# Kernel tuning notes

Hardware: AMD Instinct MI355X
Metric: run time of the kernel (lower is better)

## Reference

```python
import jax, jax.numpy as jnp
import numpy as np

B, T, E, H = 8, 1024, 1024, 16
D = E // H  # head_dim = 64


def setup_inputs() -> dict:
    key = jax.random.key(0)
    ks = jax.random.split(key, 11)
    s = 1.0 / np.sqrt(E)
    inp = {
        'query': jax.random.normal(ks[0], (B, T, E), jnp.float32),
        'key': jax.random.normal(ks[1], (B, T, E), jnp.float32),
        'value': jax.random.normal(ks[2], (B, T, E), jnp.float32),
        'Wq': jax.random.uniform(ks[3], (E, E), jnp.float32, -s, s),
        'bq': jax.random.uniform(ks[4], (E,), jnp.float32, -s, s),
        'Wk': jax.random.uniform(ks[5], (E, E), jnp.float32, -s, s),
        'bk': jax.random.uniform(ks[6], (E,), jnp.float32, -s, s),
        'Wv': jax.random.uniform(ks[7], (E, E), jnp.float32, -s, s),
        'bv': jax.random.uniform(ks[8], (E,), jnp.float32, -s, s),
        'Wo': jax.random.uniform(ks[9], (E, E), jnp.float32, -s, s),
        'bo': jax.random.uniform(ks[10], (E,), jnp.float32, -s, s),
    }
    return inp


def reference(query, key, value, Wq, bq, Wk, bk, Wv, bv, Wo, bo):
    scale = np.sqrt(D).astype(np.float32)
    # projections: Linear applies x @ W.T + b (torch convention); W shape (out,in)
    q = (query @ Wq.T + bq).reshape(B, T, H, D).transpose(0, 2, 1, 3)  # (B,H,Tq,D)
    k = (key @ Wk.T + bk).reshape(B, T, H, D).transpose(0, 2, 1, 3)    # (B,H,Tk,D)
    v = (value @ Wv.T + bv).reshape(B, T, H, D).transpose(0, 2, 1, 3)  # (B,H,Tk,D)
    scores = jnp.einsum('bhqd,bhkd->bhqk', q, k) / scale
    attn = jax.nn.softmax(scores, axis=-1)  # dropout = identity (eval)
    out = jnp.einsum('bhqk,bhkd->bhqd', attn, v)
    out = out.transpose(0, 2, 1, 3).reshape(B, T, E)
    return out @ Wo.T + bo
```

## Files before the change

kernel.cpp:

```cpp
#include <hip/hip_runtime.h>
#include <stdint.h>

#define BB 8
#define TT 1024
#define EE 1024
#define HH 16
#define DD 64

#define L2E8 0.18033688011112042f

typedef __attribute__((ext_vector_type(8))) __bf16 bf16x8;
typedef __attribute__((ext_vector_type(4))) float f32x4;
typedef __attribute__((ext_vector_type(4))) unsigned short ushort4v;
typedef __attribute__((ext_vector_type(4))) unsigned int uint4v;

__device__ __forceinline__ unsigned short f2bf(float f) {
  unsigned int u = __float_as_uint(f);
  u += 0x7fffu + ((u >> 16) & 1u);
  return (unsigned short)(u >> 16);
}

__device__ __forceinline__ unsigned int pk2t(float a, float b) {
  return __builtin_amdgcn_perm(__float_as_uint(b) + 0x8000u,
                               __float_as_uint(a) + 0x8000u, 0x07060302u);
}

__device__ __forceinline__ f32x4 mfma_16x16x32(bf16x8 a, bf16x8 b, f32x4 c) {
  return __builtin_amdgcn_mfma_f32_16x16x32_bf16(a, b, c, 0, 0, 0);
}

__device__ __forceinline__ void async_ld16(const unsigned short* g, unsigned short* l) {
  __builtin_amdgcn_global_load_lds(
      (const __attribute__((address_space(1))) void*)g,
      (__attribute__((address_space(3))) void*)l, 16, 0, 0);
}

__global__ __launch_bounds__(256) void cast_all(
    const float* __restrict__ xq, const float* __restrict__ xk, const float* __restrict__ xv,
    const float* __restrict__ wq, const float* __restrict__ wk,
    const float* __restrict__ wv, const float* __restrict__ wo,
    unsigned short* __restrict__ ws) {
  int blk = blockIdx.x;
  const float* src; size_t dstoff; int rel;
  if (blk < 4096)       { src = xq; dstoff = 0;        rel = blk; }
  else if (blk < 8192)  { src = xk; dstoff = 8388608;  rel = blk - 4096; }
  else if (blk < 12288) { src = xv; dstoff = 16777216; rel = blk - 8192; }
  else if (blk < 12800) { src = wq; dstoff = 25165824; rel = blk - 12288; }
  else if (blk < 13312) { src = wk; dstoff = 26214400; rel = blk - 12800; }
  else if (blk < 13824) { src = wv; dstoff = 27262976; rel = blk - 13312; }
  else                  { src = wo; dstoff = 28311552; rel = blk - 13824; }
  size_t base = (size_t)rel * 2048 + (size_t)threadIdx.x * 8;
  float4 a = *(const float4*)(src + base);
  float4 b = *(const float4*)(src + base + 4);
  ushort4v o0, o1;
  o0.x = f2bf(a.x); o0.y = f2bf(a.y); o0.z = f2bf(a.z); o0.w = f2bf(a.w);
  o1.x = f2bf(b.x); o1.y = f2bf(b.y); o1.z = f2bf(b.z); o1.w = f2bf(b.w);
  *(ushort4v*)(ws + dstoff + base) = o0;
  *(ushort4v*)(ws + dstoff + base + 4) = o1;
}

__global__ __launch_bounds__(256, 3) void fused_proj(
    const unsigned short* __restrict__ xq, const unsigned short* __restrict__ xk,
    const unsigned short* __restrict__ xv, const unsigned short* __restrict__ wq,
    const unsigned short* __restrict__ wk, const unsigned short* __restrict__ wv,
    const float* __restrict__ bq, const float* __restrict__ bk, const float* __restrict__ bv,
    unsigned short* __restrict__ Qb, unsigned short* __restrict__ Kb,
    unsigned short* __restrict__ Vtb) {
  const int id = blockIdx.x;
  const int tid = threadIdx.x;
  const int wave = tid >> 6, lane = tid & 63;
  const int quad = lane >> 4, l16 = lane & 15;
  const int wr = wave >> 1, wc = wave & 1;

  const unsigned short *A, *W;
  const float* bias;
  int mode, m0, n0;
  size_t zoff = 0;
  if (id < 512) {
    mode = 0; A = xq; W = wq; bias = bq;
    m0 = (id >> 3) * 128; n0 = (id & 7) * 128;
  } else if (id < 1024) {
    int t = id - 512;
    mode = 1; A = xk; W = wk; bias = bk;
    m0 = (t >> 3) * 128; n0 = (t & 7) * 128;
  } else {
    int t = id - 1024;
    int z = t >> 6;
    mode = 2; A = wv; W = xv + (size_t)z * 1048576; bias = bv;
    m0 = ((t >> 3) & 7) * 128; n0 = (t & 7) * 128;
    zoff = (size_t)z * 1048576;
  }

  __shared__ __align__(16) unsigned short As[128 * 64];
  __shared__ __align__(16) unsigned short Bs[128 * 64];

  const unsigned short* Wb = W + (size_t)n0 * 1024;

  f32x4 acc[4][4];
#pragma unroll
  for (int i = 0; i < 4; ++i)
#pragma unroll
    for (int j = 0; j < 4; ++j) acc[i][j] = (f32x4){0.f, 0.f, 0.f, 0.f};

  const int row_s = tid >> 3, kc_s = (tid & 7) * 8;
  for (int kt = 0; kt < 16; ++kt) {
    const unsigned short* Akt = A + (size_t)m0 * 1024 + kt * 64;
    const unsigned short* Wkt = Wb + kt * 64;
#pragma unroll
    for (int i = 0; i < 4; ++i) {
      int g = i * 256 + tid;
      int row = row_s + i * 32;
      async_ld16(Akt + (size_t)row * 1024 + kc_s, As + g * 8);
      async_ld16(Wkt + (size_t)row * 1024 + kc_s, Bs + g * 8);
    }
    __syncthreads();
#pragma unroll
    for (int ks = 0; ks < 2; ++ks) {
      bf16x8 af[4], bfv[4];
      int ko = ks * 32 + quad * 8;
#pragma unroll
      for (int i = 0; i < 4; ++i)
        af[i] = *(const bf16x8*)(As + (wr * 64 + i * 16 + l16) * 64 + ko);
#pragma unroll
      for (int j = 0; j < 4; ++j)
        bfv[j] = *(const bf16x8*)(Bs + (wc * 64 + j * 16 + l16) * 64 + ko);
#pragma unroll
      for (int i = 0; i < 4; ++i)
#pragma unroll
        for (int j = 0; j < 4; ++j) acc[i][j] = mfma_16x16x32(af[i], bfv[j], acc[i][j]);
    }
    __syncthreads();
  }

  if (mode == 2) {
    size_t base = zoff;
    const int nxor = ((((l16 >> 2) + 1) & 2) ? 12 : 0);
#pragma unroll
    for (int i = 0; i < 4; ++i)
#pragma unroll
      for (int r = 0; r < 4; ++r) {
        int m = m0 + wr * 64 + i * 16 + quad * 4 + r;
        float bm = bias[m];
#pragma unroll
        for (int j = 0; j < 4; ++j) {
          int n = (n0 + wc * 64 + j * 16 + l16) ^ nxor;
          Vtb[base + (size_t)m * 1024 + n] = f2bf(acc[i][j][r] + bm);
        }
      }
  } else {
    unsigned short* Out = (mode == 0) ? Qb : Kb;
    const float scale = (mode == 0) ? L2E8 : 1.0f;
#pragma unroll
    for (int j = 0; j < 4; ++j) {
      int n = n0 + wc * 64 + j * 16 + l16;
      float bn = bias[n];
      int h = n >> 6, d = n & 63;
#pragma unroll
      for (int i = 0; i < 4; ++i)
#pragma unroll
        for (int r = 0; r < 4; ++r) {
          int m = m0 + wr * 64 + i * 16 + quad * 4 + r;
          int b = m >> 10, t = m & 1023;
          float v = (acc[i][j][r] + bn) * scale;
          Out[((size_t)((b << 4) + h) * 1024 + t) * 64 + d] = f2bf(v);
        }
    }
  }
}

__global__ __launch_bounds__(256, 4) void gemm_out(
    const unsigned short* __restrict__ A, const unsigned short* __restrict__ Wm,
    const float* __restrict__ bias, float* __restrict__ Cout) {
  const int tid = threadIdx.x;
  const int wave = tid >> 6, lane = tid & 63;
  const int quad = lane >> 4, l16 = lane & 15;
  const int wr = wave >> 1, wc = wave & 1;
  const int n0 = blockIdx.x * 128;
  const int m0 = blockIdx.y * 64;

  __shared__ __align__(16) unsigned short As[64 * 64];
  __shared__ __align__(16) unsigned short Bs[128 * 64];

  const unsigned short* Wb = Wm + (size_t)n0 * 1024;

  f32x4 acc[2][4];
#pragma unroll
  for (int i = 0; i < 2; ++i)
#pragma unroll
    for (int j = 0; j < 4; ++j) acc[i][j] = (f32x4){0.f, 0.f, 0.f, 0.f};

  const int row_s = tid >> 3, kc_s = (tid & 7) * 8;
  for (int kt = 0; kt < 16; ++kt) {
    const unsigned short* Akt =
        A + (size_t)(m0 >> 10) * 1048576 + (size_t)kt * 65536 + (size_t)(m0 & 1023) * 64;
    const unsigned short* Wkt = Wb + kt * 64;
#pragma unroll
    for (int i = 0; i < 2; ++i) {
      int row = row_s + i * 32;
      async_ld16(Akt + (size_t)row * 64 + kc_s, As + (i * 256 + tid) * 8);
    }
#pragma unroll
    for (int i = 0; i < 4; ++i) {
      int row = row_s + i * 32;
      async_ld16(Wkt + (size_t)row * 1024 + kc_s, Bs + (i * 256 + tid) * 8);
    }
    __syncthreads();
#pragma unroll
    for (int ks = 0; ks < 2; ++ks) {
      bf16x8 af[2], bfv[4];
      int ko = ks * 32 + quad * 8;
#pragma unroll
      for (int i = 0; i < 2; ++i)
        af[i] = *(const bf16x8*)(As + (wr * 32 + i * 16 + l16) * 64 + ko);
#pragma unroll
      for (int j = 0; j < 4; ++j)
        bfv[j] = *(const bf16x8*)(Bs + (wc * 64 + j * 16 + l16) * 64 + ko);
#pragma unroll
      for (int i = 0; i < 2; ++i)
#pragma unroll
        for (int j = 0; j < 4; ++j) acc[i][j] = mfma_16x16x32(af[i], bfv[j], acc[i][j]);
    }
    __syncthreads();
  }

#pragma unroll
  for (int j = 0; j < 4; ++j) {
    int n = n0 + wc * 64 + j * 16 + l16;
    float bn = bias[n];
#pragma unroll
    for (int i = 0; i < 2; ++i)
#pragma unroll
      for (int r = 0; r < 4; ++r) {
        int m = m0 + wr * 32 + i * 16 + quad * 4 + r;
        Cout[(size_t)m * 1024 + n] = acc[i][j][r] + bn;
      }
  }
}

__global__ __launch_bounds__(256) void attn(
    const unsigned short* __restrict__ Q,
    const unsigned short* __restrict__ K,
    const unsigned short* __restrict__ Vt,
    unsigned short* __restrict__ O) {
  const int bh = blockIdx.x;
  const int tid = threadIdx.x;
  const int wave = tid >> 6, lane = tid & 63;
  const int quad = lane >> 4, l16 = lane & 15;
  const int q0 = blockIdx.y * 64 + wave * 16;
  const size_t bhTD = (size_t)bh * (TT * DD);
  const unsigned short* Qb = Q + bhTD;
  const unsigned short* Kb = K + bhTD;
  const unsigned short* Vb = Vt + bhTD;

  __shared__ __align__(16) unsigned short Ks[64 * 64];
  __shared__ __align__(16) unsigned short Vs[64 * 64];

  bf16x8 q_lo = *(const bf16x8*)(Qb + (size_t)(q0 + l16) * 64 + quad * 8);
  bf16x8 q_hi = *(const bf16x8*)(Qb + (size_t)(q0 + l16) * 64 + 32 + quad * 8);

  uint4v ou; ou.x = ou.y = ou.z = ou.w = 0x3F803F80u;
  const bf16x8 ones = __builtin_bit_cast(bf16x8, ou);

  f32x4 o_acc[4];
#pragma unroll
  for (int dd = 0; dd < 4; ++dd) o_acc[dd] = (f32x4){0.f, 0.f, 0.f, 0.f};
  f32x4 acc5 = (f32x4){0.f, 0.f, 0.f, 0.f};
  const bool lo_half = (quad < 2);

  const int srow = tid >> 3;
  const int schunk = tid & 7;

  for (int it = 0; it < 16; ++it) {
    const int kv0 = it * 64;
#pragma unroll
    for (int i = 0; i < 2; ++i) {
      int row = srow + i * 32;
      int gc = schunk ^ (row & 7);
      async_ld16(Kb + (size_t)(kv0 + row) * 64 + gc * 8, Ks + (row * 8 + schunk) * 8);
      async_ld16(Vb + (size_t)row * 1024 + kv0 + gc * 8, Vs + (row * 8 + schunk) * 8);
    }
    __syncthreads();

    f32x4 f[4];
#pragma unroll
    for (int c = 0; c < 2; ++c) {
      const int r0 = c * 32 + l16;
      const int r1 = r0 + 16;
      const int sw = r0 & 7;
      bf16x8 k00 = *(const bf16x8*)(Ks + (r0 * 8 + (quad ^ sw)) * 8);
      bf16x8 k01 = *(const bf16x8*)(Ks + (r0 * 8 + ((quad + 4) ^ sw)) * 8);
      bf16x8 k10 = *(const bf16x8*)(Ks + (r1 * 8 + (quad ^ sw)) * 8);
      bf16x8 k11 = *(const bf16x8*)(Ks + (r1 * 8 + ((quad + 4) ^ sw)) * 8);
      f32x4 a = (f32x4){0.f, 0.f, 0.f, 0.f};
      f32x4 b = (f32x4){0.f, 0.f, 0.f, 0.f};
      a = mfma_16x16x32(k00, q_lo, a);
      a = mfma_16x16x32(k01, q_hi, a);
      b = mfma_16x16x32(k10, q_lo, b);
      b = mfma_16x16x32(k11, q_hi, b);
      f[2 * c] = a; f[2 * c + 1] = b;
    }

#pragma unroll
    for (int c = 0; c < 2; ++c) {
      f32x4 f0 = f[2 * c], f1 = f[2 * c + 1];
      float p0 = __builtin_amdgcn_exp2f(f0[0]), p1 = __builtin_amdgcn_exp2f(f0[1]);
      float p2 = __builtin_amdgcn_exp2f(f0[2]), p3 = __builtin_amdgcn_exp2f(f0[3]);
      float p4 = __builtin_amdgcn_exp2f(f1[0]), p5 = __builtin_amdgcn_exp2f(f1[1]);
      float p6 = __builtin_amdgcn_exp2f(f1[2]), p7 = __builtin_amdgcn_exp2f(f1[3]);
      unsigned int u01 = pk2t(p0, p1), u23 = pk2t(p2, p3);
      unsigned int u45 = pk2t(p4, p5), u67 = pk2t(p6, p7);
      unsigned int pu01 = __shfl_xor(u01, 32), pu23 = __shfl_xor(u23, 32);
      unsigned int pu45 = __shfl_xor(u45, 32), pu67 = __shfl_xor(u67, 32);
      uint4v av;
      av.x = lo_half ? u01 : pu45;
      av.y = lo_half ? u23 : pu67;
      av.z = lo_half ? pu01 : u45;
      av.w = lo_half ? pu23 : u67;
      bf16x8 ap = __builtin_bit_cast(bf16x8, av);
      acc5 = mfma_16x16x32(ap, ones, acc5);
#pragma unroll
      for (int dd = 0; dd < 4; ++dd) {
        int vr = dd * 16 + l16;
        bf16x8 bv = *(const bf16x8*)(Vs + (vr * 8 + ((c * 4 + quad) ^ (vr & 7))) * 8);
        o_acc[dd] = mfma_16x16x32(ap, bv, o_acc[dd]);
      }
    }
    __syncthreads();
  }
#pragma unroll
  for (int r = 0; r < 4; ++r) {
    float invr = 1.f / acc5[r];
    int trow = q0 + quad * 4 + r;
#pragma unroll
    for (int dd = 0; dd < 4; ++dd)
      O[bhTD + (size_t)trow * 64 + dd * 16 + l16] = f2bf(o_acc[dd][r] * invr);
  }
}

extern "C" void kernel_launch(void* const* d_in, const int* in_sizes, int n_in,
                              void* d_out, int out_size, void* d_ws, size_t ws_size,
                              hipStream_t stream) {
  const float* xq = (const float*)d_in[0];
  const float* xk = (const float*)d_in[1];
  const float* xv = (const float*)d_in[2];
  const float* Wq = (const float*)d_in[3];
  const float* bq = (const float*)d_in[4];
  const float* Wk = (const float*)d_in[5];
  const float* bk = (const float*)d_in[6];
  const float* Wv = (const float*)d_in[7];
  const float* bv = (const float*)d_in[8];
  const float* Wo = (const float*)d_in[9];
  const float* bo = (const float*)d_in[10];

  unsigned short* ws = (unsigned short*)d_ws;
  unsigned short* xq_b = ws;
  unsigned short* xk_b = ws + 8388608;
  unsigned short* xv_b = ws + 16777216;
  unsigned short* wq_b = ws + 25165824;
  unsigned short* wk_b = ws + 26214400;
  unsigned short* wv_b = ws + 27262976;
  unsigned short* wo_b = ws + 28311552;
  unsigned short* Qbuf = ws + 29360128;
  unsigned short* Kbuf = ws + 37748736;
  unsigned short* Vtb  = ws + 46137344;
  unsigned short* Obuf = ws + 54525952;

  cast_all<<<14336, 256, 0, stream>>>(xq, xk, xv, Wq, Wk, Wv, Wo, ws);

  fused_proj<<<1536, 256, 0, stream>>>(xq_b, xk_b, xv_b, wq_b, wk_b, wv_b,
                                       bq, bk, bv, Qbuf, Kbuf, Vtb);
  attn<<<dim3(128, 16), 256, 0, stream>>>(Qbuf, Kbuf, Vtb, Obuf);
  gemm_out<<<dim3(8, 128), 256, 0, stream>>>(Obuf, wo_b, bo, (float*)d_out);
}
```

Measured before the change: 317.2 us.

## Double-buffer attention KV tiles, coarsen cast kernel, and swizzle GEMM block order

The attention kernel now double-buffers K/V tiles in LDS, issuing the async load of the next tile before computing on the current one, so global-load latency overlaps with MFMA work. The cast kernel processes four chunks per thread and packs pairs into bf16 with the cheaper truncating-round pk2t, cutting the block count fourfold. The projection and output GEMMs remap block indices so groups of 8 consecutive blocks share the same N tile across 8 M tiles, which is meant to improve L2 reuse. The extra LDS buffer doubles attention shared memory and may lower occupancy, and pk2t rounds ties differently from the original f2bf.

```diff
diff --git a/kernel.cpp b/kernel.cpp
--- a/kernel.cpp
+++ b/kernel.cpp
@@ -42,21 +42,24 @@
     unsigned short* __restrict__ ws) {
   int blk = blockIdx.x;
   const float* src; size_t dstoff; int rel;
-  if (blk < 4096)       { src = xq; dstoff = 0;        rel = blk; }
-  else if (blk < 8192)  { src = xk; dstoff = 8388608;  rel = blk - 4096; }
-  else if (blk < 12288) { src = xv; dstoff = 16777216; rel = blk - 8192; }
-  else if (blk < 12800) { src = wq; dstoff = 25165824; rel = blk - 12288; }
-  else if (blk < 13312) { src = wk; dstoff = 26214400; rel = blk - 12800; }
-  else if (blk < 13824) { src = wv; dstoff = 27262976; rel = blk - 13312; }
-  else                  { src = wo; dstoff = 28311552; rel = blk - 13824; }
-  size_t base = (size_t)rel * 2048 + (size_t)threadIdx.x * 8;
-  float4 a = *(const float4*)(src + base);
-  float4 b = *(const float4*)(src + base + 4);
-  ushort4v o0, o1;
-  o0.x = f2bf(a.x); o0.y = f2bf(a.y); o0.z = f2bf(a.z); o0.w = f2bf(a.w);
-  o1.x = f2bf(b.x); o1.y = f2bf(b.y); o1.z = f2bf(b.z); o1.w = f2bf(b.w);
-  *(ushort4v*)(ws + dstoff + base) = o0;
-  *(ushort4v*)(ws + dstoff + base + 4) = o1;
+  if (blk < 1024)       { src = xq; dstoff = 0;        rel = blk; }
+  else if (blk < 2048)  { src = xk; dstoff = 8388608;  rel = blk - 1024; }
+  else if (blk < 3072)  { src = xv; dstoff = 16777216; rel = blk - 2048; }
+  else if (blk < 3200)  { src = wq; dstoff = 25165824; rel = blk - 3072; }
+  else if (blk < 3328)  { src = wk; dstoff = 26214400; rel = blk - 3200; }
+  else if (blk < 3456)  { src = wv; dstoff = 27262976; rel = blk - 3328; }
+  else                  { src = wo; dstoff = 28311552; rel = blk - 3456; }
+  size_t base = (size_t)rel * 8192 + (size_t)threadIdx.x * 8;
+#pragma unroll
+  for (int c = 0; c < 4; ++c) {
+    size_t off = base + (size_t)c * 2048;
+    float4 a = *(const float4*)(src + off);
+    float4 b = *(const float4*)(src + off + 4);
+    uint4v o;
+    o.x = pk2t(a.x, a.y); o.y = pk2t(a.z, a.w);
+    o.z = pk2t(b.x, b.y); o.w = pk2t(b.z, b.w);
+    *(uint4v*)(ws + dstoff + off) = o;
+  }
 }
 
 __global__ __launch_bounds__(256, 3) void fused_proj(
@@ -77,17 +80,18 @@
   int mode, m0, n0;
   size_t zoff = 0;
   if (id < 512) {
+    int g = id;
     mode = 0; A = xq; W = wq; bias = bq;
-    m0 = (id >> 3) * 128; n0 = (id & 7) * 128;
+    m0 = ((g & 7) | ((g >> 6) << 3)) * 128; n0 = ((g >> 3) & 7) * 128;
   } else if (id < 1024) {
-    int t = id - 512;
+    int g = id - 512;
     mode = 1; A = xk; W = wk; bias = bk;
-    m0 = (t >> 3) * 128; n0 = (t & 7) * 128;
+    m0 = ((g & 7) | ((g >> 6) << 3)) * 128; n0 = ((g >> 3) & 7) * 128;
   } else {
-    int t = id - 1024;
-    int z = t >> 6;
+    int g = id - 1024;
+    int z = g >> 6;
     mode = 2; A = wv; W = xv + (size_t)z * 1048576; bias = bv;
-    m0 = ((t >> 3) & 7) * 128; n0 = (t & 7) * 128;
+    m0 = (g & 7) * 128; n0 = ((g >> 3) & 7) * 128;
     zoff = (size_t)z * 1048576;
   }
 
@@ -171,12 +175,13 @@
 __global__ __launch_bounds__(256, 4) void gemm_out(
     const unsigned short* __restrict__ A, const unsigned short* __restrict__ Wm,
     const float* __restrict__ bias, float* __restrict__ Cout) {
+  const int g = blockIdx.x;
   const int tid = threadIdx.x;
   const int wave = tid >> 6, lane = tid & 63;
   const int quad = lane >> 4, l16 = lane & 15;
   const int wr = wave >> 1, wc = wave & 1;
-  const int n0 = blockIdx.x * 128;
-  const int m0 = blockIdx.y * 64;
+  const int n0 = ((g >> 3) & 7) * 128;
+  const int m0 = ((g & 7) | ((g >> 6) << 3)) * 64;
 
   __shared__ __align__(16) unsigned short As[64 * 64];
   __shared__ __align__(16) unsigned short Bs[128 * 64];
@@ -252,8 +257,8 @@
   const unsigned short* Kb = K + bhTD;
   const unsigned short* Vb = Vt + bhTD;
 
-  __shared__ __align__(16) unsigned short Ks[64 * 64];
-  __shared__ __align__(16) unsigned short Vs[64 * 64];
+  __shared__ __align__(16) unsigned short Ks[2][64 * 64];
+  __shared__ __align__(16) unsigned short Vs[2][64 * 64];
 
   bf16x8 q_lo = *(const bf16x8*)(Qb + (size_t)(q0 + l16) * 64 + quad * 8);
   bf16x8 q_hi = *(const bf16x8*)(Qb + (size_t)(q0 + l16) * 64 + 32 + quad * 8);
@@ -270,16 +275,25 @@
   const int srow = tid >> 3;
   const int schunk = tid & 7;
 
+#define STAGE(IT, BUF)                                                                 \
+  {                                                                                    \
+    const int kv0s = (IT) * 64;                                                        \
+    _Pragma("unroll") for (int i = 0; i < 2; ++i) {                                    \
+      int row = srow + i * 32;                                                         \
+      int gc = schunk ^ (row & 7);                                                     \
+      async_ld16(Kb + (size_t)(kv0s + row) * 64 + gc * 8,                              \
+                 Ks[BUF] + (row * 8 + schunk) * 8);                                    \
+      async_ld16(Vb + (size_t)row * 1024 + kv0s + gc * 8,                              \
+                 Vs[BUF] + (row * 8 + schunk) * 8);                                    \
+    }                                                                                  \
+  }
+
+  STAGE(0, 0);
+  __syncthreads();
+
   for (int it = 0; it < 16; ++it) {
-    const int kv0 = it * 64;
-#pragma unroll
-    for (int i = 0; i < 2; ++i) {
-      int row = srow + i * 32;
-      int gc = schunk ^ (row & 7);
-      async_ld16(Kb + (size_t)(kv0 + row) * 64 + gc * 8, Ks + (row * 8 + schunk) * 8);
-      async_ld16(Vb + (size_t)row * 1024 + kv0 + gc * 8, Vs + (row * 8 + schunk) * 8);
-    }
-    __syncthreads();
+    const int buf = it & 1;
+    if (it < 15) STAGE(it + 1, buf ^ 1);
 
     f32x4 f[4];
 #pragma unroll
@@ -287,10 +301,10 @@
       const int r0 = c * 32 + l16;
       const int r1 = r0 + 16;
       const int sw = r0 & 7;
-      bf16x8 k00 = *(const bf16x8*)(Ks + (r0 * 8 + (quad ^ sw)) * 8);
-      bf16x8 k01 = *(const bf16x8*)(Ks + (r0 * 8 + ((quad + 4) ^ sw)) * 8);
-      bf16x8 k10 = *(const bf16x8*)(Ks + (r1 * 8 + (quad ^ sw)) * 8);
-      bf16x8 k11 = *(const bf16x8*)(Ks + (r1 * 8 + ((quad + 4) ^ sw)) * 8);
+      bf16x8 k00 = *(const bf16x8*)(Ks[buf] + (r0 * 8 + (quad ^ sw)) * 8);
+      bf16x8 k01 = *(const bf16x8*)(Ks[buf] + (r0 * 8 + ((quad + 4) ^ sw)) * 8);
+      bf16x8 k10 = *(const bf16x8*)(Ks[buf] + (r1 * 8 + (quad ^ sw)) * 8);
+      bf16x8 k11 = *(const bf16x8*)(Ks[buf] + (r1 * 8 + ((quad + 4) ^ sw)) * 8);
       f32x4 a = (f32x4){0.f, 0.f, 0.f, 0.f};
       f32x4 b = (f32x4){0.f, 0.f, 0.f, 0.f};
       a = mfma_16x16x32(k00, q_lo, a);
@@ -321,12 +335,14 @@
 #pragma unroll
       for (int dd = 0; dd < 4; ++dd) {
         int vr = dd * 16 + l16;
-        bf16x8 bv = *(const bf16x8*)(Vs + (vr * 8 + ((c * 4 + quad) ^ (vr & 7))) * 8);
+        bf16x8 bv = *(const bf16x8*)(Vs[buf] + (vr * 8 + ((c * 4 + quad) ^ (vr & 7))) * 8);
         o_acc[dd] = mfma_16x16x32(ap, bv, o_acc[dd]);
       }
     }
     __syncthreads();
   }
+#undef STAGE
+
 #pragma unroll
   for (int r = 0; r < 4; ++r) {
     float invr = 1.f / acc5[r];
@@ -365,10 +381,10 @@
   unsigned short* Vtb  = ws + 46137344;
   unsigned short* Obuf = ws + 54525952;
 
-  cast_all<<<14336, 256, 0, stream>>>(xq, xk, xv, Wq, Wk, Wv, Wo, ws);
+  cast_all<<<3584, 256, 0, stream>>>(xq, xk, xv, Wq, Wk, Wv, Wo, ws);
 
   fused_proj<<<1536, 256, 0, stream>>>(xq_b, xk_b, xv_b, wq_b, wk_b, wv_b,
                                        bq, bk, bv, Qbuf, Kbuf, Vtb);
   attn<<<dim3(128, 16), 256, 0, stream>>>(Qbuf, Kbuf, Vtb, Obuf);
-  gemm_out<<<dim3(8, 128), 256, 0, stream>>>(Obuf, wo_b, bo, (float*)d_out);
-}
+  gemm_out<<<1024, 256, 0, stream>>>(Obuf, wo_b, bo, (float*)d_out);
+}
```

Result: no change. 319.4 us (+0.7%).
